# Kernel tuning notes

Measured on AMD Instinct MI355X. Metric: run time of the kernel, lower is better.

Reference implementation:

```python
import jax, jax.numpy as jnp
import numpy as np

N, C, T, V = 128, 64, 128, 25   # batch, channels (in==out), frames, joints
R = 8                            # rel_channels = in_channels // rel_reduction
H = 12                           # SE hidden dim for joint attention (~V//2)


def setup_inputs() -> dict:
    key = jax.random.key(0)
    ks = jax.random.split(key, 8)
    w = lambda shape, k: jax.random.normal(k, shape, jnp.float32) * 0.05
    return {
        "x": jax.random.normal(ks[0], (N, C, T, V), jnp.float32),
        "A": jax.random.normal(ks[1], (V, V), jnp.float32) * 0.1,
        "w1": w((R, C), ks[2]), "b1": jnp.zeros((R,), jnp.float32),
        "w2": w((R, C), ks[3]), "b2": jnp.zeros((R,), jnp.float32),
        "w4": w((C, R), ks[4]), "b4": jnp.zeros((C,), jnp.float32),
        "se_w1": w((H, V), ks[5]), "se_b1": jnp.zeros((H,), jnp.float32),
        "se_w2": w((V, H), ks[6]), "se_b2": jnp.zeros((V,), jnp.float32),
    }


def reference(x, A, w1, b1, w2, b2, w4, b4, se_w1, se_b1, se_w2, se_b2):
    alpha = 1.0
    # conv1/conv2 are 1x1 convs; mean over T commutes with the linear map,
    # so pool first then project (saves a (N,R,T,V) intermediate).
    xm = x.mean(axis=2)                                     # (N,C,V)
    x1 = jnp.einsum('rc,ncv->nrv', w1, xm) + b1[None, :, None]
    x2 = jnp.einsum('rc,ncv->nrv', w2, xm) + b2[None, :, None]
    # channel-wise relation: broadcast diff + tanh  -> (N,R,V,V)
    rel = jnp.tanh(x1[:, :, :, None] - x2[:, :, None, :])
    # conv4 (1x1) lifts R->C, scale by alpha, add static adjacency
    Adyn = jnp.einsum('or,nruv->nouv', w4, rel) + b4[None, :, None, None]
    Adyn = Adyn * alpha + A[None, None]                     # (N,C,V,V)
    # DRJointSpa: SE attention over joints (pool C,T -> FC -> ReLU -> FC -> sigmoid)
    s = x.mean(axis=(1, 2))                                 # (N,V)
    h = jax.nn.relu(jnp.einsum('hv,nv->nh', se_w1, s) + se_b1)
    a = jax.nn.sigmoid(jnp.einsum('vh,nh->nv', se_w2, h) + se_b2)
    x3 = x * a[:, None, None, :]                            # (N,C,T,V)
    # per-channel graph aggregation over joints
    return jnp.einsum('ncuv,nctv->nctu', Adyn, x3)
```

## Files before the change

### kernel.cpp

```cpp
#include <hip/hip_runtime.h>
#include <hip/hip_bf16.h>

#define NN 128
#define CC 64
#define TT 128
#define VV 25
#define RR 8
#define HH 12
#define RELP 28
#define RELR (VV*RELP)
#define RELN (RR*RELR)
#define KP 40

typedef __attribute__((ext_vector_type(8))) short short8;
typedef __attribute__((ext_vector_type(4))) float f32x4;

__device__ __forceinline__ unsigned int f2bf(float f) {
    unsigned int u = __builtin_bit_cast(unsigned int, f);
    return (u + 0x7FFFu + ((u >> 16) & 1u)) >> 16;
}
__device__ __forceinline__ float bf2f(unsigned int b) {
    return __builtin_bit_cast(float, b << 16);
}

__global__ __launch_bounds__(256) void kA_tmean(const float* __restrict__ x,
                                                float* __restrict__ xm) {
    const int blk = blockIdx.x;
    const int tid = threadIdx.x;
    __shared__ float st[TT * VV];
    __shared__ float ps[8 * VV];

    const float4* xb4 = (const float4*)(x + (size_t)blk * (TT * VV));
    float4* st4 = (float4*)st;
    for (int i = tid; i < (TT * VV) / 4; i += 256) st4[i] = xb4[i];
    __syncthreads();

    if (tid < 200) {
        const int v = tid % VV, tseg = tid / VV;
        float s = 0.f;
        const int base = tseg * 16 * VV + v;
#pragma unroll
        for (int i = 0; i < 16; i++) s += st[base + i * VV];
        ps[tseg * VV + v] = s;
    }
    __syncthreads();
    if (tid < VV) {
        float s = 0.f;
#pragma unroll
        for (int k = 0; k < 8; k++) s += ps[k * VV + tid];
        xm[(size_t)blk * VV + tid] = s * (1.f / TT);
    }
}

__global__ __launch_bounds__(256) void kB_small(
    const float* __restrict__ xm,
    const float* __restrict__ w1, const float* __restrict__ b1,
    const float* __restrict__ w2, const float* __restrict__ b2,
    const float* __restrict__ sw1, const float* __restrict__ sb1,
    const float* __restrict__ sw2, const float* __restrict__ sb2,
    float* __restrict__ a_out, float* __restrict__ rel_out) {
    const int n = blockIdx.x;
    const int tid = threadIdx.x;
    __shared__ float lxm[CC * VV];
    __shared__ float ls[VV];
    __shared__ float lh[HH];
    __shared__ float l1[RR * VV];
    __shared__ float l2[RR * VV];

    for (int i = tid; i < CC * VV; i += 256) lxm[i] = xm[(size_t)n * CC * VV + i];
    __syncthreads();

    if (tid < VV) {
        float s = 0.f;
        for (int c = 0; c < CC; c++) s += lxm[c * VV + tid];
        ls[tid] = s * (1.f / CC);
    }
    if (tid < RR * VV) {
        int r = tid / VV, v = tid % VV;
        float s1 = b1[r], s2 = b2[r];
        for (int c = 0; c < CC; c++) {
            float xv = lxm[c * VV + v];
            s1 += w1[r * CC + c] * xv;
            s2 += w2[r * CC + c] * xv;
        }
        l1[tid] = s1;
        l2[tid] = s2;
    }
    __syncthreads();

    if (tid < HH) {
        float h = sb1[tid];
        for (int v = 0; v < VV; v++) h += sw1[tid * VV + v] * ls[v];
        lh[tid] = fmaxf(h, 0.f);
    }
    __syncthreads();

    if (tid < VV) {
        float z = sb2[tid];
        for (int j = 0; j < HH; j++) z += sw2[tid * HH + j] * lh[j];
        a_out[(size_t)n * VV + tid] = 1.f / (1.f + expf(-z));
    }

    for (int idx = tid; idx < RELN; idx += 256) {
        int r = idx / RELR;
        int rem = idx - r * RELR;
        int u = rem / RELP;
        int v = rem - u * RELP;
        float val = 0.f;
        if (v < VV) val = tanhf(l1[r * VV + u] - l2[r * VV + v]);
        rel_out[(size_t)n * RELN + idx] = val;
    }
}

__global__ __launch_bounds__(256) void kC_main(
    const float* __restrict__ x, const float* __restrict__ A,
    const float* __restrict__ w4, const float* __restrict__ b4,
    const float* __restrict__ rel, const float* __restrict__ av,
    float* __restrict__ out) {
    const int blk = blockIdx.x;
    const int n = blk >> 6;
    const int c = blk & (CC - 1);
    const int tid = threadIdx.x;

    __shared__ __align__(16) unsigned short xsb[2][TT * KP];
    __shared__ __align__(16) unsigned short adb[2][32 * KP];
    float* os = (float*)&xsb[0][0];

    const float* xg = x + (size_t)blk * (TT * VV);

    {
        int t = tid / 13;
        int p = tid - t * 13;
#pragma unroll
        for (int it = 0; it < 7; ++it) {
            if (it < 6 || t < TT) {
                const float* row = xg + t * VV + 2 * p;
                float f0 = row[0];
                float f1 = row[(p < 12) ? 1 : 0];
                if (p >= 12) f1 = 0.f;
                unsigned int h0 = f2bf(f0);
                unsigned int l0 = f2bf(f0 - bf2f(h0));
                unsigned int h1 = f2bf(f1);
                unsigned int l1 = f2bf(f1 - bf2f(h1));
                *(unsigned int*)&xsb[0][t * KP + 2 * p] = h0 | (h1 << 16);
                *(unsigned int*)&xsb[1][t * KP + 2 * p] = l0 | (l1 << 16);
            }
            p += 9; t += 19;
            if (p >= 13) { p -= 13; ++t; }
        }
        for (int i = tid; i < TT * 3; i += 256) {
            int tt = i / 3, q = i - (i / 3) * 3;
            *(unsigned int*)&xsb[0][tt * KP + 26 + 2 * q] = 0u;
            *(unsigned int*)&xsb[1][tt * KP + 26 + 2 * q] = 0u;
        }
    }

    {
        float w4r[RR];
#pragma unroll
        for (int r = 0; r < RR; r++) w4r[r] = w4[c * RR + r];
        const float b4c = b4[c];

        if (tid < VV * 7) {
            const int u = tid / 7;
            const int v0 = (tid - u * 7) * 4;
            const float* rp = rel + (size_t)n * RELN + u * RELP + v0;
            float s0 = b4c, s1 = b4c, s2 = b4c, s3 = b4c;
#pragma unroll
            for (int r = 0; r < RR; r++) {
                const float4 rq = *(const float4*)(rp + r * RELR);
                s0 += w4r[r] * rq.x;
                s1 += w4r[r] * rq.y;
                s2 += w4r[r] * rq.z;
                s3 += w4r[r] * rq.w;
            }
            const int c0 = v0;
            const int c1 = min(v0 + 1, VV - 1);
            const int c2 = min(v0 + 2, VV - 1);
            const int c3 = min(v0 + 3, VV - 1);
            const float* Ar = A + u * VV;
            const float* avp = av + (size_t)n * VV;
            float o0 = (s0 + Ar[c0]) * avp[c0];
            float o1 = (s1 + Ar[c1]) * avp[c1];
            float o2 = (s2 + Ar[c2]) * avp[c2];
            float o3 = (s3 + Ar[c3]) * avp[c3];
            unsigned int h0 = f2bf(o0), h1 = f2bf(o1), h2 = f2bf(o2), h3 = f2bf(o3);
            unsigned int l0 = f2bf(o0 - bf2f(h0));
            unsigned int l1 = f2bf(o1 - bf2f(h1));
            unsigned int l2 = f2bf(o2 - bf2f(h2));
            unsigned int l3 = f2bf(o3 - bf2f(h3));
            *(unsigned int*)&adb[0][u * KP + v0]     = h0 | (h1 << 16);
            *(unsigned int*)&adb[0][u * KP + v0 + 2] = h2 | (h3 << 16);
            *(unsigned int*)&adb[1][u * KP + v0]     = l0 | (l1 << 16);
            *(unsigned int*)&adb[1][u * KP + v0 + 2] = l2 | (l3 << 16);
        }
        if (tid < 25 * 6) {
            int u = tid / 6, q = tid - (tid / 6) * 6;
            *(unsigned int*)&adb[0][u * KP + 28 + 2 * q] = 0u;
            *(unsigned int*)&adb[1][u * KP + 28 + 2 * q] = 0u;
        }
        for (int i = tid; i < 7 * 20; i += 256) {
            int rr2 = i / 20, cc2 = i - (i / 20) * 20;
            *(unsigned int*)&adb[0][(VV + rr2) * KP + 2 * cc2] = 0u;
            *(unsigned int*)&adb[1][(VV + rr2) * KP + 2 * cc2] = 0u;
        }
    }
    __syncthreads();

    const int wid = tid >> 6;
    const int lane = tid & 63;
    const int fr = lane & 15;
    const int fk = (lane >> 4) * 8;

    f32x4 acc[2][2] = {};
    short8 ah[2], al[2], bh[2], bl[2];
#pragma unroll
    for (int mi = 0; mi < 2; ++mi) {
        const int m = (wid * 2 + mi) * 16 + fr;
        ah[mi] = *(const short8*)&xsb[0][m * KP + fk];
        al[mi] = *(const short8*)&xsb[1][m * KP + fk];
    }
#pragma unroll
    for (int ni = 0; ni < 2; ++ni) {
        const int nn2 = ni * 16 + fr;
        bh[ni] = *(const short8*)&adb[0][nn2 * KP + fk];
        bl[ni] = *(const short8*)&adb[1][nn2 * KP + fk];
    }
#pragma unroll
    for (int mi = 0; mi < 2; ++mi)
#pragma unroll
        for (int ni = 0; ni < 2; ++ni) {
            acc[mi][ni] = __builtin_amdgcn_mfma_f32_16x16x32_bf16(ah[mi], bh[ni], acc[mi][ni], 0, 0, 0);
            acc[mi][ni] = __builtin_amdgcn_mfma_f32_16x16x32_bf16(ah[mi], bl[ni], acc[mi][ni], 0, 0, 0);
            acc[mi][ni] = __builtin_amdgcn_mfma_f32_16x16x32_bf16(al[mi], bh[ni], acc[mi][ni], 0, 0, 0);
        }
    __syncthreads();

#pragma unroll
    for (int mi = 0; mi < 2; ++mi) {
        const int tb = (wid * 2 + mi) * 16 + (lane >> 4) * 4;
#pragma unroll
        for (int ni = 0; ni < 2; ++ni) {
            const int u = ni * 16 + fr;
            if (u < VV) {
#pragma unroll
                for (int r = 0; r < 4; ++r)
                    os[(tb + r) * VV + u] = acc[mi][ni][r];
            }
        }
    }
    __syncthreads();

    float4* ob4 = (float4*)(out + (size_t)blk * (TT * VV));
    const float4* os4 = (const float4*)os;
    ob4[tid]       = os4[tid];
    ob4[tid + 256] = os4[tid + 256];
    ob4[tid + 512] = os4[tid + 512];
    if (tid < 32) ob4[tid + 768] = os4[tid + 768];
}

extern "C" void kernel_launch(void* const* d_in, const int* in_sizes, int n_in,
                              void* d_out, int out_size, void* d_ws, size_t ws_size,
                              hipStream_t stream) {
    const float* x   = (const float*)d_in[0];
    const float* A   = (const float*)d_in[1];
    const float* w1  = (const float*)d_in[2];
    const float* b1  = (const float*)d_in[3];
    const float* w2  = (const float*)d_in[4];
    const float* b2  = (const float*)d_in[5];
    const float* w4  = (const float*)d_in[6];
    const float* b4  = (const float*)d_in[7];
    const float* sw1 = (const float*)d_in[8];
    const float* sb1 = (const float*)d_in[9];
    const float* sw2 = (const float*)d_in[10];
    const float* sb2 = (const float*)d_in[11];
    float* out = (float*)d_out;

    float* ws = (float*)d_ws;
    float* xm  = ws;
    float* a_s = xm + (size_t)NN * CC * VV;
    float* rel = a_s + (size_t)NN * VV;

    kA_tmean<<<NN * CC, 256, 0, stream>>>(x, xm);
    kB_small<<<NN, 256, 0, stream>>>(xm, w1, b1, w2, b2, sw1, sb1, sw2, sb2, a_s, rel);
    kC_main<<<NN * CC, 256, 0, stream>>>(x, A, w4, b4, rel, a_s, out);
}
```

Baseline: 229.9 us.

## Split main kernel over time halves and spread small kernel across more blocks

The main aggregation kernel now launches two blocks per (n,c), each handling 64 frames, which halves its shared memory and per-wave MFMA work and adds a launch-bounds occupancy hint. The adjacency tile is rebuilt redundantly in both halves. The small kernel is split into one block per (n,r) for the tanh relation plus separate blocks for the SE attention, so it uses many more blocks than the single block per batch item it had before. The aim is more parallelism and occupancy, at the cost of duplicated adjacency construction and more, smaller blocks.

Result: slower. 236.9 us (+3.0%).

```diff
diff --git a/kernel.cpp b/kernel.cpp
--- a/kernel.cpp
+++ b/kernel.cpp
@@ -11,6 +11,7 @@
 #define RELR (VV*RELP)
 #define RELN (RR*RELR)
 #define KP 40
+#define THALF 64
 
 typedef __attribute__((ext_vector_type(8))) short short8;
 typedef __attribute__((ext_vector_type(4))) float f32x4;
@@ -59,100 +60,95 @@
     const float* __restrict__ sw1, const float* __restrict__ sb1,
     const float* __restrict__ sw2, const float* __restrict__ sb2,
     float* __restrict__ a_out, float* __restrict__ rel_out) {
-    const int n = blockIdx.x;
+    const int bid = blockIdx.x;
     const int tid = threadIdx.x;
     __shared__ float lxm[CC * VV];
-    __shared__ float ls[VV];
+    __shared__ float l1[VV];
+    __shared__ float l2[VV];
     __shared__ float lh[HH];
-    __shared__ float l1[RR * VV];
-    __shared__ float l2[RR * VV];
-
-    for (int i = tid; i < CC * VV; i += 256) lxm[i] = xm[(size_t)n * CC * VV + i];
-    __syncthreads();
-
-    if (tid < VV) {
-        float s = 0.f;
-        for (int c = 0; c < CC; c++) s += lxm[c * VV + tid];
-        ls[tid] = s * (1.f / CC);
-    }
-    if (tid < RR * VV) {
-        int r = tid / VV, v = tid % VV;
-        float s1 = b1[r], s2 = b2[r];
-        for (int c = 0; c < CC; c++) {
-            float xv = lxm[c * VV + v];
-            s1 += w1[r * CC + c] * xv;
-            s2 += w2[r * CC + c] * xv;
-        }
-        l1[tid] = s1;
-        l2[tid] = s2;
-    }
-    __syncthreads();
-
-    if (tid < HH) {
-        float h = sb1[tid];
-        for (int v = 0; v < VV; v++) h += sw1[tid * VV + v] * ls[v];
-        lh[tid] = fmaxf(h, 0.f);
-    }
-    __syncthreads();
-
-    if (tid < VV) {
-        float z = sb2[tid];
-        for (int j = 0; j < HH; j++) z += sw2[tid * HH + j] * lh[j];
-        a_out[(size_t)n * VV + tid] = 1.f / (1.f + expf(-z));
-    }
-
-    for (int idx = tid; idx < RELN; idx += 256) {
-        int r = idx / RELR;
-        int rem = idx - r * RELR;
-        int u = rem / RELP;
-        int v = rem - u * RELP;
-        float val = 0.f;
-        if (v < VV) val = tanhf(l1[r * VV + u] - l2[r * VV + v]);
-        rel_out[(size_t)n * RELN + idx] = val;
-    }
-}
-
-__global__ __launch_bounds__(256) void kC_main(
+
+    if (bid < NN * RR) {
+        const int n = bid >> 3;
+        const int r = bid & 7;
+        for (int i = tid; i < CC * VV; i += 256) lxm[i] = xm[(size_t)n * CC * VV + i];
+        __syncthreads();
+
+        if (tid < 2 * VV) {
+            const int which = tid / VV;
+            const int u = tid - which * VV;
+            const float* w = which ? w2 : w1;
+            float s = which ? b2[r] : b1[r];
+            for (int c = 0; c < CC; c++) s += w[r * CC + c] * lxm[c * VV + u];
+            if (which) l2[u] = s; else l1[u] = s;
+        }
+        __syncthreads();
+
+        float* ro = rel_out + (size_t)n * RELN + (size_t)r * RELR;
+        for (int idx = tid; idx < RELR; idx += 256) {
+            int u = idx / RELP, v = idx - u * RELP;
+            ro[idx] = (v < VV) ? tanhf(l1[u] - l2[v]) : 0.f;
+        }
+    } else {
+        const int n = bid - NN * RR;
+        for (int i = tid; i < CC * VV; i += 256) lxm[i] = xm[(size_t)n * CC * VV + i];
+        __syncthreads();
+
+        if (tid < VV) {
+            float s = 0.f;
+            for (int c = 0; c < CC; c++) s += lxm[c * VV + tid];
+            l1[tid] = s * (1.f / CC);
+        }
+        __syncthreads();
+        if (tid < HH) {
+            float h = sb1[tid];
+            for (int v = 0; v < VV; v++) h += sw1[tid * VV + v] * l1[v];
+            lh[tid] = fmaxf(h, 0.f);
+        }
+        __syncthreads();
+        if (tid < VV) {
+            float z = sb2[tid];
+            for (int j = 0; j < HH; j++) z += sw2[tid * HH + j] * lh[j];
+            a_out[(size_t)n * VV + tid] = 1.f / (1.f + expf(-z));
+        }
+    }
+}
+
+__global__ __launch_bounds__(256, 4) void kC_main(
     const float* __restrict__ x, const float* __restrict__ A,
     const float* __restrict__ w4, const float* __restrict__ b4,
     const float* __restrict__ rel, const float* __restrict__ av,
     float* __restrict__ out) {
-    const int blk = blockIdx.x;
-    const int n = blk >> 6;
-    const int c = blk & (CC - 1);
+    const int bid = blockIdx.x;
+    const int nc = bid >> 1;
+    const int half = bid & 1;
+    const int n = nc >> 6;
+    const int c = nc & (CC - 1);
     const int tid = threadIdx.x;
 
-    __shared__ __align__(16) unsigned short xsb[2][TT * KP];
+    __shared__ __align__(16) unsigned short xsb[2][THALF * KP];
     __shared__ __align__(16) unsigned short adb[2][32 * KP];
     float* os = (float*)&xsb[0][0];
 
-    const float* xg = x + (size_t)blk * (TT * VV);
-
-    {
-        int t = tid / 13;
-        int p = tid - t * 13;
-#pragma unroll
-        for (int it = 0; it < 7; ++it) {
-            if (it < 6 || t < TT) {
-                const float* row = xg + t * VV + 2 * p;
-                float f0 = row[0];
-                float f1 = row[(p < 12) ? 1 : 0];
-                if (p >= 12) f1 = 0.f;
-                unsigned int h0 = f2bf(f0);
-                unsigned int l0 = f2bf(f0 - bf2f(h0));
-                unsigned int h1 = f2bf(f1);
-                unsigned int l1 = f2bf(f1 - bf2f(h1));
-                *(unsigned int*)&xsb[0][t * KP + 2 * p] = h0 | (h1 << 16);
-                *(unsigned int*)&xsb[1][t * KP + 2 * p] = l0 | (l1 << 16);
-            }
-            p += 9; t += 19;
-            if (p >= 13) { p -= 13; ++t; }
-        }
-        for (int i = tid; i < TT * 3; i += 256) {
-            int tt = i / 3, q = i - (i / 3) * 3;
-            *(unsigned int*)&xsb[0][tt * KP + 26 + 2 * q] = 0u;
-            *(unsigned int*)&xsb[1][tt * KP + 26 + 2 * q] = 0u;
-        }
+    const float* xg = x + ((size_t)nc * TT + half * THALF) * VV;
+
+    for (int idx = tid; idx < THALF * 13; idx += 256) {
+        const int t = idx / 13;
+        const int p = idx - t * 13;
+        const float* row = xg + t * VV + 2 * p;
+        float f0 = row[0];
+        float f1 = row[(p < 12) ? 1 : 0];
+        if (p >= 12) f1 = 0.f;
+        unsigned int h0 = f2bf(f0);
+        unsigned int l0 = f2bf(f0 - bf2f(h0));
+        unsigned int h1 = f2bf(f1);
+        unsigned int l1 = f2bf(f1 - bf2f(h1));
+        *(unsigned int*)&xsb[0][t * KP + 2 * p] = h0 | (h1 << 16);
+        *(unsigned int*)&xsb[1][t * KP + 2 * p] = l0 | (l1 << 16);
+    }
+    if (tid < THALF * 3) {
+        int tt = tid / 3, q = tid - (tid / 3) * 3;
+        *(unsigned int*)&xsb[0][tt * KP + 26 + 2 * q] = 0u;
+        *(unsigned int*)&xsb[1][tt * KP + 26 + 2 * q] = 0u;
     }
 
     {
@@ -199,8 +195,8 @@
             *(unsigned int*)&adb[0][u * KP + 28 + 2 * q] = 0u;
             *(unsigned int*)&adb[1][u * KP + 28 + 2 * q] = 0u;
         }
-        for (int i = tid; i < 7 * 20; i += 256) {
-            int rr2 = i / 20, cc2 = i - (i / 20) * 20;
+        if (tid < 7 * 20) {
+            int rr2 = tid / 20, cc2 = tid - (tid / 20) * 20;
             *(unsigned int*)&adb[0][(VV + rr2) * KP + 2 * cc2] = 0u;
             *(unsigned int*)&adb[1][(VV + rr2) * KP + 2 * cc2] = 0u;
         }
@@ -211,52 +207,41 @@
     const int lane = tid & 63;
     const int fr = lane & 15;
     const int fk = (lane >> 4) * 8;
-
-    f32x4 acc[2][2] = {};
-    short8 ah[2], al[2], bh[2], bl[2];
+    const int ni = wid & 1;
+    const int mb = (wid >> 1) * 2;
+
+    const short8 bh = *(const short8*)&adb[0][(ni * 16 + fr) * KP + fk];
+    const short8 bl = *(const short8*)&adb[1][(ni * 16 + fr) * KP + fk];
+    f32x4 acc[2] = {};
 #pragma unroll
     for (int mi = 0; mi < 2; ++mi) {
-        const int m = (wid * 2 + mi) * 16 + fr;
-        ah[mi] = *(const short8*)&xsb[0][m * KP + fk];
-        al[mi] = *(const short8*)&xsb[1][m * KP + fk];
-    }
-#pragma unroll
-    for (int ni = 0; ni < 2; ++ni) {
-        const int nn2 = ni * 16 + fr;
-        bh[ni] = *(const short8*)&adb[0][nn2 * KP + fk];
-        bl[ni] = *(const short8*)&adb[1][nn2 * KP + fk];
-    }
-#pragma unroll
-    for (int mi = 0; mi < 2; ++mi)
-#pragma unroll
-        for (int ni = 0; ni < 2; ++ni) {
-            acc[mi][ni] = __builtin_amdgcn_mfma_f32_16x16x32_bf16(ah[mi], bh[ni], acc[mi][ni], 0, 0, 0);
-            acc[mi][ni] = __builtin_amdgcn_mfma_f32_16x16x32_bf16(ah[mi], bl[ni], acc[mi][ni], 0, 0, 0);
-            acc[mi][ni] = __builtin_amdgcn_mfma_f32_16x16x32_bf16(al[mi], bh[ni], acc[mi][ni], 0, 0, 0);
-        }
-    __syncthreads();
-
-#pragma unroll
-    for (int mi = 0; mi < 2; ++mi) {
-        const int tb = (wid * 2 + mi) * 16 + (lane >> 4) * 4;
-#pragma unroll
-        for (int ni = 0; ni < 2; ++ni) {
-            const int u = ni * 16 + fr;
-            if (u < VV) {
+        const int m = (mb + mi) * 16 + fr;
+        const short8 ah = *(const short8*)&xsb[0][m * KP + fk];
+        const short8 al = *(const short8*)&xsb[1][m * KP + fk];
+        acc[mi] = __builtin_amdgcn_mfma_f32_16x16x32_bf16(ah, bh, acc[mi], 0, 0, 0);
+        acc[mi] = __builtin_amdgcn_mfma_f32_16x16x32_bf16(ah, bl, acc[mi], 0, 0, 0);
+        acc[mi] = __builtin_amdgcn_mfma_f32_16x16x32_bf16(al, bh, acc[mi], 0, 0, 0);
+    }
+    __syncthreads();
+
+    {
+        const int u = ni * 16 + fr;
+        if (u < VV) {
+#pragma unroll
+            for (int mi = 0; mi < 2; ++mi) {
+                const int tb = (mb + mi) * 16 + (lane >> 4) * 4;
 #pragma unroll
                 for (int r = 0; r < 4; ++r)
-                    os[(tb + r) * VV + u] = acc[mi][ni][r];
+                    os[(tb + r) * VV + u] = acc[mi][r];
             }
         }
     }
     __syncthreads();
 
-    float4* ob4 = (float4*)(out + (size_t)blk * (TT * VV));
+    float4* ob4 = (float4*)(out + ((size_t)nc * TT + half * THALF) * VV);
     const float4* os4 = (const float4*)os;
-    ob4[tid]       = os4[tid];
-    ob4[tid + 256] = os4[tid + 256];
-    ob4[tid + 512] = os4[tid + 512];
-    if (tid < 32) ob4[tid + 768] = os4[tid + 768];
+    ob4[tid] = os4[tid];
+    if (tid < 144) ob4[tid + 256] = os4[tid + 256];
 }
 
 extern "C" void kernel_launch(void* const* d_in, const int* in_sizes, int n_in,
@@ -282,6 +267,6 @@
     float* rel = a_s + (size_t)NN * VV;
 
     kA_tmean<<<NN * CC, 256, 0, stream>>>(x, xm);
-    kB_small<<<NN, 256, 0, stream>>>(xm, w1, b1, w2, b2, sw1, sb1, sw2, sb2, a_s, rel);
-    kC_main<<<NN * CC, 256, 0, stream>>>(x, A, w4, b4, rel, a_s, out);
-}
+    kB_small<<<NN * RR + NN, 256, 0, stream>>>(xm, w1, b1, w2, b2, sw1, sb1, sw2, sb2, a_s, rel);
+    kC_main<<<NN * CC * 2, 256, 0, stream>>>(x, A, w4, b4, rel, a_s, out);
+}
```
